# Performance work log

Measured on AMD Instinct MI355X. Metric: run time of the kernel, lower is better.

## Reference

```python
import jax, jax.numpy as jnp
import numpy as np

N = 50000

def gcn_conv(x, W, b, src, dst, n):
    # x: [N, Fin], W: [Fin, Fout]; PyG GCNConv: transform then sym-normalized aggregate (self-loops included in src/dst)
    h = x @ W  # [N, Fout]
    deg = jax.ops.segment_sum(jnp.ones_like(dst, dtype=h.dtype), dst, num_segments=n)
    inv_sqrt = jnp.where(deg > 0, jax.lax.rsqrt(deg), 0.0)
    norm = inv_sqrt[src] * inv_sqrt[dst]  # [E+N]
    msg = h[src] * norm[:, None]
    out = jax.ops.segment_sum(msg, dst, num_segments=n)
    return out + b


def setup_inputs() -> dict:
    key = jax.random.key(0)
    ks = jax.random.split(key, 8)
    d_in, d_h, n_exp, E = 64, 64, 16, 800000
    x = jax.random.normal(ks[0], (N, d_in), dtype=jnp.float32)
    edge_index = jax.random.randint(ks[1], (2, E), 0, N, dtype=jnp.int64)
    s = 1.0 / np.sqrt(d_in)
    W1 = jax.random.uniform(ks[2], (d_in, d_h), minval=-s, maxval=s, dtype=jnp.float32)
    b1 = jnp.zeros((d_h,), jnp.float32)
    W2 = jax.random.uniform(ks[3], (d_h, d_h), minval=-s, maxval=s, dtype=jnp.float32)
    b2 = jnp.zeros((d_h,), jnp.float32)
    Wc = jax.random.uniform(ks[4], (d_h, n_exp), minval=-s, maxval=s, dtype=jnp.float32)
    bc = jnp.zeros((n_exp,), jnp.float32)
    return {"x": x, "edge_index": edge_index, "W1": W1, "b1": b1, "W2": W2, "b2": b2, "Wc": Wc, "bc": bc}


def reference(x, edge_index, W1, b1, W2, b2, Wc, bc):
    # add self-loops once (PyG GCNConv default add_self_loops=True)
    loops = jnp.arange(N, dtype=edge_index.dtype)
    src = jnp.concatenate([edge_index[0], loops])
    dst = jnp.concatenate([edge_index[1], loops])
    h = jax.nn.relu(gcn_conv(x, W1, b1, src, dst, N))
    # dropout is identity in eval mode
    h = jax.nn.relu(gcn_conv(h, W2, b2, src, dst, N))
    return h @ Wc + bc
```

## Files before the change

kernel.cpp:

```cpp
#include <hip/hip_runtime.h>
#include <hip/hip_fp16.h>


#define FDIM 64
#define NCLS 16
#define TILE 2048

__global__ __launch_bounds__(256) void k_histB(const int* __restrict__ dst, int E,
                                               int* __restrict__ H) {
    __shared__ int h[256];
    int t = threadIdx.x, blk = blockIdx.x;
    h[t] = 0;
    __syncthreads();
    int i0 = blk * TILE;
#pragma unroll
    for (int k = 0; k < TILE / 256; ++k) {
        int i = i0 + k * 256 + t;
        if (i < E) atomicAdd(&h[dst[i] >> 8], 1);
    }
    __syncthreads();
    H[blk * 256 + t] = h[t];
}

__global__ __launch_bounds__(512) void k_scanH(int* __restrict__ H, int nblk, int* __restrict__ btot) {
    __shared__ int s[512];
    int t = threadIdx.x, b = blockIdx.x;
    int v = (t < nblk) ? H[t * 256 + b] : 0;
    s[t] = v;
    __syncthreads();
    for (int off = 1; off < 512; off <<= 1) {
        int add = (t >= off) ? s[t - off] : 0;
        __syncthreads();
        s[t] += add;
        __syncthreads();
    }
    if (t < nblk) H[t * 256 + b] = s[t] - v;
    if (t == 511) btot[b] = s[511];
}

__global__ __launch_bounds__(256) void k_scatA(const int* __restrict__ src, const int* __restrict__ dst,
                                               int E, const int* __restrict__ H,
                                               const int* __restrict__ btot, int nb,
                                               unsigned* __restrict__ tmp) {
    __shared__ int s[256];
    __shared__ int Hb[256];
    __shared__ int c2[256];
    int t = threadIdx.x, blk = blockIdx.x;
    int v = (t < nb) ? btot[t] : 0;
    s[t] = v;
    __syncthreads();
    for (int off = 1; off < 256; off <<= 1) {
        int add = (t >= off) ? s[t - off] : 0;
        __syncthreads();
        s[t] += add;
        __syncthreads();
    }
    Hb[t] = (s[t] - v) + H[blk * 256 + t];
    c2[t] = 0;
    __syncthreads();
    int i0 = blk * TILE;
#pragma unroll
    for (int k = 0; k < TILE / 256; ++k) {
        int i = i0 + k * 256 + t;
        if (i < E) {
            int sv = src[i], d = dst[i];
            int b = d >> 8;
            unsigned rec = ((unsigned)(d & 255) << 16) | (unsigned)sv;
            int pos = Hb[b] + atomicAdd(&c2[b], 1);
            tmp[pos] = rec;
        }
    }
}

#define COLCAP 8192
__global__ __launch_bounds__(256) void k_binB(const unsigned* __restrict__ tmp,
                                              const int* __restrict__ btot, int nb,
                                              int n, int E, int* __restrict__ row_ptr,
                                              float* __restrict__ inv,
                                              unsigned short* __restrict__ col) {
    __shared__ int dcnt[256], s[256], cur[256];
    __shared__ unsigned short colbuf[COLCAP];
    int t = threadIdx.x, b = blockIdx.x;
    int v = (t < nb) ? btot[t] : 0;
    s[t] = v;
    __syncthreads();
    for (int off = 1; off < 256; off <<= 1) {
        int add = (t >= off) ? s[t - off] : 0;
        __syncthreads();
        s[t] += add;
        __syncthreads();
    }
    __shared__ int baseS;
    if (t == b) baseS = s[t] - v;
    dcnt[t] = 0;
    __syncthreads();
    int base = baseS;
    int cntE = btot[b];
    int node0 = b << 8;
    int nn = min(256, n - node0);
    for (int i = t; i < cntE; i += 256) atomicAdd(&dcnt[tmp[base + i] >> 16], 1);
    __syncthreads();
    int deg = dcnt[t];
    s[t] = deg;
    __syncthreads();
    for (int off = 1; off < 256; off <<= 1) {
        int add = (t >= off) ? s[t - off] : 0;
        __syncthreads();
        s[t] += add;
        __syncthreads();
    }
    int excl = s[t] - deg;
    if (t < nn) {
        row_ptr[node0 + t] = base + excl;
        inv[node0 + t] = rsqrtf((float)(deg + 1));
    }
    if (b == 0 && t == 0) row_ptr[n] = E;
    cur[t] = excl;
    __syncthreads();
    for (int i = t; i < cntE; i += 256) {
        unsigned r = tmp[base + i];
        int pos = atomicAdd(&cur[r >> 16], 1);
        unsigned short vv = (unsigned short)(r & 0xFFFFu);
        if (pos < COLCAP) colbuf[pos] = vv;
        else col[base + pos] = vv;
    }
    __syncthreads();
    int lim = min(cntE, COLCAP);
    for (int i = t; i < lim; i += 256) col[base + i] = colbuf[i];
}

__global__ __launch_bounds__(256) void k_gemm64(const float* __restrict__ X, const float* __restrict__ W,
                                                const float* __restrict__ inv, __half* __restrict__ Yh, int n) {
    __shared__ float Ws[FDIM * FDIM];
    int t = threadIdx.x;
    for (int i = t; i < FDIM * FDIM; i += 256) Ws[i] = W[i];
    __syncthreads();
    int idx = blockIdx.x * 256 + t;
    int row = idx >> 2;
    int cg = (idx & 3) * 16;
    if (row >= n) return;
    const float4* xr = (const float4*)(X + row * FDIM);
    float4 xv[16];
#pragma unroll
    for (int i = 0; i < 16; ++i) xv[i] = xr[i];
    float acc[16];
#pragma unroll
    for (int c = 0; c < 16; ++c) acc[c] = 0.f;
#pragma unroll
    for (int i = 0; i < 16; ++i) {
        float xs[4] = {xv[i].x, xv[i].y, xv[i].z, xv[i].w};
#pragma unroll
        for (int j = 0; j < 4; ++j) {
            float xk = xs[j];
            const float* wr = &Ws[(i * 4 + j) * FDIM + cg];
#pragma unroll
            for (int c = 0; c < 16; ++c) acc[c] += xk * wr[c];
        }
    }
    float iv = inv[row];
    unsigned u[8];
#pragma unroll
    for (int i = 0; i < 8; ++i) {
        __half2 hp = __floats2half2_rn(acc[2 * i] * iv, acc[2 * i + 1] * iv);
        u[i] = *(unsigned*)&hp;
    }
    uint4* yo = (uint4*)(Yh + (size_t)row * FDIM + cg);
    yo[0] = make_uint4(u[0], u[1], u[2], u[3]);
    yo[1] = make_uint4(u[4], u[5], u[6], u[7]);
}

__global__ __launch_bounds__(256) void k_aggF1(const __half* __restrict__ Ph, const float* __restrict__ inv,
                                               const int* __restrict__ row_ptr,
                                               const unsigned short* __restrict__ col,
                                               const float* __restrict__ bias,
                                               const float* __restrict__ W2,
                                               __half* __restrict__ P2, int n) {
    __shared__ float W2s[FDIM * FDIM];
    __shared__ float rbuf[16][FDIM + 1];
    int t = threadIdx.x;
    for (int i = t; i < FDIM * FDIM; i += 256) W2s[i] = W2[i];
    int lane = t & 63;
    int sub = lane >> 4;
    int fl = lane & 15;
    int wid = t >> 6;
    int nl = wid * 4 + sub;
    int node = blockIdx.x * 16 + nl;
    bool alive = node < n;
    int nodeC = alive ? node : (n - 1);
    float iv = inv[nodeC];
    const uint2* Pq = (const uint2*)Ph;
    uint2 selfq = Pq[(size_t)nodeC * 16 + fl];
    float2 sf0 = __half22float2(*(__half2*)&selfq.x);
    float2 sf1 = __half22float2(*(__half2*)&selfq.y);
    float4 acc = make_float4(sf0.x, sf0.y, sf1.x, sf1.y);
    int s = row_ptr[nodeC];
    int e = alive ? row_ptr[nodeC + 1] : s;
    int dmax = e - s;
    dmax = max(dmax, __shfl_xor(dmax, 16, 64));
    dmax = max(dmax, __shfl_xor(dmax, 32, 64));
    for (int j = 0; j < dmax; j += 8) {
        int c[8];
        float wk[8];
        uint2 q[8];
#pragma unroll
        for (int k = 0; k < 8; ++k) {
            int jj = s + j + k;
            bool ok = jj < e;
            c[k] = col[ok ? jj : s];
            wk[k] = ok ? 1.f : 0.f;
        }
#pragma unroll
        for (int k = 0; k < 8; ++k) q[k] = Pq[(size_t)c[k] * 16 + fl];
#pragma unroll
        for (int k = 0; k < 8; ++k) {
            float2 f0 = __half22float2(*(__half2*)&q[k].x);
            float2 f1 = __half22float2(*(__half2*)&q[k].y);
            acc.x = fmaf(wk[k], f0.x, acc.x);
            acc.y = fmaf(wk[k], f0.y, acc.y);
            acc.z = fmaf(wk[k], f1.x, acc.z);
            acc.w = fmaf(wk[k], f1.y, acc.w);
        }
    }
    float4 bb = ((const float4*)bias)[fl];
    rbuf[nl][fl * 4 + 0] = fmaxf(fmaf(iv, acc.x, bb.x), 0.f);
    rbuf[nl][fl * 4 + 1] = fmaxf(fmaf(iv, acc.y, bb.y), 0.f);
    rbuf[nl][fl * 4 + 2] = fmaxf(fmaf(iv, acc.z, bb.z), 0.f);
    rbuf[nl][fl * 4 + 3] = fmaxf(fmaf(iv, acc.w, bb.w), 0.f);
    __syncthreads();
    int nl2 = t >> 4;
    int cg = t & 15;
    int node2 = blockIdx.x * 16 + nl2;
    const float* rr = rbuf[nl2];
    float a0 = 0.f, a1 = 0.f, a2 = 0.f, a3 = 0.f;
#pragma unroll
    for (int i = 0; i < FDIM; ++i) {
        float xk = rr[i];
        const float* wv = &W2s[i * FDIM + cg * 4];
        a0 = fmaf(xk, wv[0], a0);
        a1 = fmaf(xk, wv[1], a1);
        a2 = fmaf(xk, wv[2], a2);
        a3 = fmaf(xk, wv[3], a3);
    }
    if (node2 < n) {
        float iv2 = inv[node2];
        __half2 h0 = __floats2half2_rn(a0 * iv2, a1 * iv2);
        __half2 h1 = __floats2half2_rn(a2 * iv2, a3 * iv2);
        uint2 val = make_uint2(*(unsigned*)&h0, *(unsigned*)&h1);
        ((uint2*)P2)[(size_t)node2 * 16 + cg] = val;
    }
}

__global__ __launch_bounds__(256) void k_aggF2(const __half* __restrict__ Ph, const float* __restrict__ inv,
                                               const int* __restrict__ row_ptr,
                                               const unsigned short* __restrict__ col,
                                               const float* __restrict__ bias,
                                               const float* __restrict__ Wc, const float* __restrict__ bc,
                                               float* __restrict__ out, int n) {
    __shared__ float WcT[NCLS * FDIM];
    int t = threadIdx.x;
    for (int i = t; i < FDIM * NCLS; i += 256) {
        int c = i & 15, f = i >> 4;
        WcT[c * FDIM + f] = Wc[i];
    }
    __syncthreads();
    int lane = t & 63;
    int sub = lane >> 4;
    int fl = lane & 15;
    int wid = t >> 6;
    int node = blockIdx.x * 16 + wid * 4 + sub;
    bool alive = node < n;
    int nodeC = alive ? node : (n - 1);
    float iv = inv[nodeC];
    const uint2* Pq = (const uint2*)Ph;
    uint2 selfq = Pq[(size_t)nodeC * 16 + fl];
    float2 sf0 = __half22float2(*(__half2*)&selfq.x);
    float2 sf1 = __half22float2(*(__half2*)&selfq.y);
    float4 acc = make_float4(sf0.x, sf0.y, sf1.x, sf1.y);
    int s = row_ptr[nodeC];
    int e = alive ? row_ptr[nodeC + 1] : s;
    int dmax = e - s;
    dmax = max(dmax, __shfl_xor(dmax, 16, 64));
    dmax = max(dmax, __shfl_xor(dmax, 32, 64));
    for (int j = 0; j < dmax; j += 8) {
        int c[8];
        float wk[8];
        uint2 q[8];
#pragma unroll
        for (int k = 0; k < 8; ++k) {
            int jj = s + j + k;
            bool ok = jj < e;
            c[k] = col[ok ? jj : s];
            wk[k] = ok ? 1.f : 0.f;
        }
#pragma unroll
        for (int k = 0; k < 8; ++k) q[k] = Pq[(size_t)c[k] * 16 + fl];
#pragma unroll
        for (int k = 0; k < 8; ++k) {
            float2 f0 = __half22float2(*(__half2*)&q[k].x);
            float2 f1 = __half22float2(*(__half2*)&q[k].y);
            acc.x = fmaf(wk[k], f0.x, acc.x);
            acc.y = fmaf(wk[k], f0.y, acc.y);
            acc.z = fmaf(wk[k], f1.x, acc.z);
            acc.w = fmaf(wk[k], f1.y, acc.w);
        }
    }
    float4 bb = ((const float4*)bias)[fl];
    float4 r;
    r.x = fmaxf(fmaf(iv, acc.x, bb.x), 0.f);
    r.y = fmaxf(fmaf(iv, acc.y, bb.y), 0.f);
    r.z = fmaxf(fmaf(iv, acc.z, bb.z), 0.f);
    r.w = fmaxf(fmaf(iv, acc.w, bb.w), 0.f);
    float part[NCLS];
#pragma unroll
    for (int c = 0; c < NCLS; ++c) {
        float4 wv = ((const float4*)(WcT + c * FDIM))[fl];
        part[c] = fmaf(r.x, wv.x, fmaf(r.y, wv.y, fmaf(r.z, wv.z, r.w * wv.w)));
    }
#pragma unroll
    for (int m = 1; m < 16; m <<= 1) {
#pragma unroll
        for (int c = 0; c < NCLS; ++c) part[c] += __shfl_xor(part[c], m, 64);
    }
    if (alive && fl < 4) {
        float4 bb2 = ((const float4*)bc)[fl];
        float4 o = make_float4(part[fl * 4 + 0] + bb2.x, part[fl * 4 + 1] + bb2.y,
                               part[fl * 4 + 2] + bb2.z, part[fl * 4 + 3] + bb2.w);
        ((float4*)out)[(size_t)node * 4 + fl] = o;
    }
}

static inline size_t align256(size_t x) { return (x + 255) & ~(size_t)255; }

extern "C" void kernel_launch(void* const* d_in, const int* in_sizes, int n_in,
                              void* d_out, int out_size, void* d_ws, size_t ws_size,
                              hipStream_t stream) {
    const float* x  = (const float*)d_in[0];
    const int*   ei = (const int*)d_in[1];
    const float* W1 = (const float*)d_in[2];
    const float* b1 = (const float*)d_in[3];
    const float* W2 = (const float*)d_in[4];
    const float* b2 = (const float*)d_in[5];
    const float* Wc = (const float*)d_in[6];
    const float* bc = (const float*)d_in[7];
    float* out = (float*)d_out;

    const int n = in_sizes[0] / FDIM;
    const int E = in_sizes[1] / 2;
    const int* src = ei;
    const int* dst = ei + E;

    const int nb = (n + 255) >> 8;
    const int nblk = (E + TILE - 1) / TILE;

    char* w = (char*)d_ws;
    size_t off = 0;
    int* H = (int*)(w + off);        off = align256(off + (size_t)nblk * 256 * 4);
    int* btot = (int*)(w + off);     off = align256(off + 256 * 4);
    int* row_ptr = (int*)(w + off);  off = align256(off + (size_t)(n + 1) * 4);
    float* inv = (float*)(w + off);  off = align256(off + (size_t)n * 4);
    unsigned* tmp = (unsigned*)(w + off);             off = align256(off + (size_t)E * 4);
    unsigned short* col = (unsigned short*)(w + off); off = align256(off + (size_t)(E + 8) * 2);
    __half* P1 = (__half*)(w + off); off = align256(off + (size_t)n * FDIM * 2);
    __half* P2 = (__half*)(w + off); off = align256(off + (size_t)n * FDIM * 2);
    (void)ws_size;

    const int nbG = (n * 4 + 255) / 256;
    const int nbA = (n + 15) / 16;

    k_histB<<<nblk, 256, 0, stream>>>(dst, E, H);
    k_scanH<<<nb, 512, 0, stream>>>(H, nblk, btot);
    k_scatA<<<nblk, 256, 0, stream>>>(src, dst, E, H, btot, nb, tmp);
    k_binB<<<nb, 256, 0, stream>>>(tmp, btot, nb, n, E, row_ptr, inv, col);

    k_gemm64<<<nbG, 256, 0, stream>>>(x, W1, inv, P1, n);
    k_aggF1<<<nbA, 256, 0, stream>>>(P1, inv, row_ptr, col, b1, W2, P2, n);
    k_aggF2<<<nbA, 256, 0, stream>>>(P2, inv, row_ptr, col, b2, Wc, bc, out, n);
}
```

Baseline: 160.4 us.

## Fuse histogram with first GEMM and apply degree scaling in bin kernel

Merges the dst histogram kernel and the first-layer X@W1 GEMM into one launch, using block-index ranges so the GEMM no longer waits on the CSR build. Because the GEMM now runs before degrees are known, the inv-sqrt(deg) row scaling moves into k_binB, which rescales each P1 row in place once its bucket's degrees are counted. This removes one launch and lets the GEMM overlap with the histogram work. In exchange, P1 makes an extra fp16 read/write round trip and is rounded to half twice.

```diff
diff --git a/kernel.cpp b/kernel.cpp
--- a/kernel.cpp
+++ b/kernel.cpp
@@ -5,21 +5,63 @@
 #define FDIM 64
 #define NCLS 16
 #define TILE 2048
-
-__global__ __launch_bounds__(256) void k_histB(const int* __restrict__ dst, int E,
-                                               int* __restrict__ H) {
-    __shared__ int h[256];
-    int t = threadIdx.x, blk = blockIdx.x;
-    h[t] = 0;
-    __syncthreads();
-    int i0 = blk * TILE;
-#pragma unroll
-    for (int k = 0; k < TILE / 256; ++k) {
-        int i = i0 + k * 256 + t;
-        if (i < E) atomicAdd(&h[dst[i] >> 8], 1);
-    }
-    __syncthreads();
-    H[blk * 256 + t] = h[t];
+#define COLCAP 8192
+
+__global__ __launch_bounds__(256) void k_hist_gemm(const int* __restrict__ dst, int E, int nblk,
+                                                   int* __restrict__ H,
+                                                   const float* __restrict__ X,
+                                                   const float* __restrict__ W,
+                                                   __half* __restrict__ Yh, int n) {
+    __shared__ float Ws[FDIM * FDIM];
+    int t = threadIdx.x, bid = blockIdx.x;
+    if (bid < nblk) {
+        int* h = (int*)Ws;
+        h[t] = 0;
+        __syncthreads();
+        int i0 = bid * TILE;
+#pragma unroll
+        for (int k = 0; k < TILE / 256; ++k) {
+            int i = i0 + k * 256 + t;
+            if (i < E) atomicAdd(&h[dst[i] >> 8], 1);
+        }
+        __syncthreads();
+        H[bid * 256 + t] = h[t];
+        return;
+    }
+    int g = bid - nblk;
+    for (int i = t; i < FDIM * FDIM; i += 256) Ws[i] = W[i];
+    __syncthreads();
+    int idx = g * 256 + t;
+    int row = idx >> 2;
+    int cgp = (idx & 3) * 16;
+    if (row >= n) return;
+    const float4* xr = (const float4*)(X + (size_t)row * FDIM);
+    float4 xv[16];
+#pragma unroll
+    for (int i = 0; i < 16; ++i) xv[i] = xr[i];
+    float acc[16];
+#pragma unroll
+    for (int c = 0; c < 16; ++c) acc[c] = 0.f;
+#pragma unroll
+    for (int i = 0; i < 16; ++i) {
+        float xs[4] = {xv[i].x, xv[i].y, xv[i].z, xv[i].w};
+#pragma unroll
+        for (int j = 0; j < 4; ++j) {
+            float xk = xs[j];
+            const float* wr = &Ws[(i * 4 + j) * FDIM + cgp];
+#pragma unroll
+            for (int c = 0; c < 16; ++c) acc[c] += xk * wr[c];
+        }
+    }
+    unsigned u[8];
+#pragma unroll
+    for (int i = 0; i < 8; ++i) {
+        __half2 hp = __floats2half2_rn(acc[2 * i], acc[2 * i + 1]);
+        u[i] = *(unsigned*)&hp;
+    }
+    uint4* yo = (uint4*)(Yh + (size_t)row * FDIM + cgp);
+    yo[0] = make_uint4(u[0], u[1], u[2], u[3]);
+    yo[1] = make_uint4(u[4], u[5], u[6], u[7]);
 }
 
 __global__ __launch_bounds__(512) void k_scanH(int* __restrict__ H, int nblk, int* __restrict__ btot) {
@@ -72,14 +114,15 @@
     }
 }
 
-#define COLCAP 8192
 __global__ __launch_bounds__(256) void k_binB(const unsigned* __restrict__ tmp,
                                               const int* __restrict__ btot, int nb,
                                               int n, int E, int* __restrict__ row_ptr,
                                               float* __restrict__ inv,
-                                              unsigned short* __restrict__ col) {
+                                              unsigned short* __restrict__ col,
+                                              __half* __restrict__ P1) {
     __shared__ int dcnt[256], s[256], cur[256];
     __shared__ unsigned short colbuf[COLCAP];
+    __shared__ int baseS;
     int t = threadIdx.x, b = blockIdx.x;
     int v = (t < nb) ? btot[t] : 0;
     s[t] = v;
@@ -90,7 +133,6 @@
         s[t] += add;
         __syncthreads();
     }
-    __shared__ int baseS;
     if (t == b) baseS = s[t] - v;
     dcnt[t] = 0;
     __syncthreads();
@@ -127,46 +169,18 @@
     __syncthreads();
     int lim = min(cntE, COLCAP);
     for (int i = t; i < lim; i += 256) col[base + i] = colbuf[i];
-}
-
-__global__ __launch_bounds__(256) void k_gemm64(const float* __restrict__ X, const float* __restrict__ W,
-                                                const float* __restrict__ inv, __half* __restrict__ Yh, int n) {
-    __shared__ float Ws[FDIM * FDIM];
-    int t = threadIdx.x;
-    for (int i = t; i < FDIM * FDIM; i += 256) Ws[i] = W[i];
-    __syncthreads();
-    int idx = blockIdx.x * 256 + t;
-    int row = idx >> 2;
-    int cg = (idx & 3) * 16;
-    if (row >= n) return;
-    const float4* xr = (const float4*)(X + row * FDIM);
-    float4 xv[16];
-#pragma unroll
-    for (int i = 0; i < 16; ++i) xv[i] = xr[i];
-    float acc[16];
-#pragma unroll
-    for (int c = 0; c < 16; ++c) acc[c] = 0.f;
-#pragma unroll
-    for (int i = 0; i < 16; ++i) {
-        float xs[4] = {xv[i].x, xv[i].y, xv[i].z, xv[i].w};
-#pragma unroll
-        for (int j = 0; j < 4; ++j) {
-            float xk = xs[j];
-            const float* wr = &Ws[(i * 4 + j) * FDIM + cg];
-#pragma unroll
-            for (int c = 0; c < 16; ++c) acc[c] += xk * wr[c];
-        }
-    }
-    float iv = inv[row];
-    unsigned u[8];
-#pragma unroll
-    for (int i = 0; i < 8; ++i) {
-        __half2 hp = __floats2half2_rn(acc[2 * i] * iv, acc[2 * i + 1] * iv);
-        u[i] = *(unsigned*)&hp;
-    }
-    uint4* yo = (uint4*)(Yh + (size_t)row * FDIM + cg);
-    yo[0] = make_uint4(u[0], u[1], u[2], u[3]);
-    yo[1] = make_uint4(u[4], u[5], u[6], u[7]);
+    uint2* P1q = (uint2*)P1;
+    for (int i = t; i < nn * 16; i += 256) {
+        int r = node0 + (i >> 4);
+        int c = i & 15;
+        float iv = rsqrtf((float)(dcnt[i >> 4] + 1));
+        uint2 q = P1q[(size_t)r * 16 + c];
+        float2 f0 = __half22float2(*(__half2*)&q.x);
+        float2 f1 = __half22float2(*(__half2*)&q.y);
+        __half2 h0 = __floats2half2_rn(f0.x * iv, f0.y * iv);
+        __half2 h1 = __floats2half2_rn(f1.x * iv, f1.y * iv);
+        P1q[(size_t)r * 16 + c] = make_uint2(*(unsigned*)&h0, *(unsigned*)&h1);
+    }
 }
 
 __global__ __launch_bounds__(256) void k_aggF1(const __half* __restrict__ Ph, const float* __restrict__ inv,
@@ -351,6 +365,8 @@
 
     const int nb = (n + 255) >> 8;
     const int nblk = (E + TILE - 1) / TILE;
+    const int nbG = (n * 4 + 255) / 256;
+    const int nbA = (n + 15) / 16;
 
     char* w = (char*)d_ws;
     size_t off = 0;
@@ -364,15 +380,10 @@
     __half* P2 = (__half*)(w + off); off = align256(off + (size_t)n * FDIM * 2);
     (void)ws_size;
 
-    const int nbG = (n * 4 + 255) / 256;
-    const int nbA = (n + 15) / 16;
-
-    k_histB<<<nblk, 256, 0, stream>>>(dst, E, H);
+    k_hist_gemm<<<nblk + nbG, 256, 0, stream>>>(dst, E, nblk, H, x, W1, P1, n);
     k_scanH<<<nb, 512, 0, stream>>>(H, nblk, btot);
     k_scatA<<<nblk, 256, 0, stream>>>(src, dst, E, H, btot, nb, tmp);
-    k_binB<<<nb, 256, 0, stream>>>(tmp, btot, nb, n, E, row_ptr, inv, col);
-
-    k_gemm64<<<nbG, 256, 0, stream>>>(x, W1, inv, P1, n);
+    k_binB<<<nb, 256, 0, stream>>>(tmp, btot, nb, n, E, row_ptr, inv, col, P1);
     k_aggF1<<<nbA, 256, 0, stream>>>(P1, inv, row_ptr, col, b1, W2, P2, n);
     k_aggF2<<<nbA, 256, 0, stream>>>(P2, inv, row_ptr, col, b2, Wc, bc, out, n);
 }
```

After: 164.1 us. 1.02x slower.
